# Kernel tuning notes

Measured on AMD Instinct MI355X. Metric: run time of the kernel, lower is better.

## Reference

```python
import jax, jax.numpy as jnp
import numpy as np
from jax import lax

T, N, E = 12, 10000, 160000
C_IN, C_H, C_OUT = 32, 64, 32
EPS = 1e-5


def _glorot(key, shape):
    fan_in, fan_out = shape[-2] if len(shape) > 1 else shape[0], shape[-1]
    s = (6.0 / (fan_in + fan_out)) ** 0.5
    return jax.random.uniform(key, shape, jnp.float32, -s, s)


def setup_inputs() -> dict:
    key = jax.random.key(0)
    ks = jax.random.split(key, 16)
    inp = {
        "x": jax.random.normal(ks[0], (T, N, C_IN), jnp.float32),
        "edge_index": jax.random.randint(ks[1], (2, E), 0, N, jnp.int32),
        "edge_weight": jax.random.uniform(ks[2], (E,), jnp.float32),
        # layer 1 (input layer): in=C_IN -> C_H
        "conv_w1": _glorot(ks[3], (C_H, C_IN, 3)) * 0.1,
        "conv_b1": jnp.zeros((C_H,), jnp.float32),
        "gamma1": jnp.ones((C_H,), jnp.float32),
        "beta1": jnp.zeros((C_H,), jnp.float32),
        "gcn_w1": _glorot(ks[4], (C_H, C_H)),
        "gcn_b1": jnp.zeros((C_H,), jnp.float32),
        # layer 2 (hidden layer): C_H -> C_H
        "conv_w2": _glorot(ks[5], (C_H, C_H, 3)) * 0.1,
        "conv_b2": jnp.zeros((C_H,), jnp.float32),
        "gamma2": jnp.ones((C_H,), jnp.float32),
        "beta2": jnp.zeros((C_H,), jnp.float32),
        "gcn_w2": _glorot(ks[6], (C_H, C_H)),
        "gcn_b2": jnp.zeros((C_H,), jnp.float32),
        # output linear: C_H -> C_OUT
        "out_w": _glorot(ks[7], (C_H, C_OUT)),
        "out_b": jnp.zeros((C_OUT,), jnp.float32),
    }
    return inp


def _stgcn_layer(x, edge_index, edge_weight, cw, cb, gamma, beta, gw, gb):
    # x: [T, N, C_in]  ->  torch.stack(x).permute(1,2,0) = [N, C_in, T]
    xs = jnp.transpose(x, (1, 2, 0))
    h = lax.conv_general_dilated(xs, cw, (1,), [(1, 1)],
                                 dimension_numbers=("NCH", "OIH", "NCH"))
    h = h + cb[None, :, None]
    # InstanceNorm1d(affine) over the temporal dim
    mu = h.mean(-1, keepdims=True)
    var = ((h - mu) ** 2).mean(-1, keepdims=True)
    h = (h - mu) * lax.rsqrt(var + EPS) * gamma[None, :, None] + beta[None, :, None]
    h = jax.nn.relu(h)
    h = jnp.transpose(h, (2, 0, 1))  # [T, N, C_out]
    # GCNConv per timestep (vectorized over T)
    src, dst = edge_index[0], edge_index[1]
    n = h.shape[1]
    deg = jnp.zeros((n,), h.dtype).at[dst].add(edge_weight) + 1.0  # self-loop weight 1
    dis = lax.rsqrt(deg)
    norm = dis[src] * edge_weight * dis[dst]  # [E]
    xw = jnp.einsum("tnc,cd->tnd", h, gw)  # [T, N, C_out]
    msg = xw[:, src, :] * norm[None, :, None]  # [T, E, C_out]
    agg = jax.vmap(lambda m: jax.ops.segment_sum(m, dst, num_segments=n))(msg)
    agg = agg + (dis * dis)[None, :, None] * xw + gb  # self loop + bias
    return agg


def reference(x, edge_index, edge_weight,
              conv_w1, conv_b1, gamma1, beta1, gcn_w1, gcn_b1,
              conv_w2, conv_b2, gamma2, beta2, gcn_w2, gcn_b2,
              out_w, out_b):
    h = _stgcn_layer(x, edge_index, edge_weight,
                     conv_w1, conv_b1, gamma1, beta1, gcn_w1, gcn_b1)
    h = _stgcn_layer(h, edge_index, edge_weight,
                     conv_w2, conv_b2, gamma2, beta2, gcn_w2, gcn_b2)
    out = jnp.einsum("tnc,co->tno", h, out_w) + out_b  # per-t linear
    return out.mean(axis=0)  # [N, C_OUT]
```

## Files before the change

kernel.cpp:

```cpp
#include <hip/hip_runtime.h>
#include <hip/hip_bf16.h>
#include <stdint.h>

#define MAXDEG 64

typedef short s16x8 __attribute__((ext_vector_type(8)));
typedef short s16x4 __attribute__((ext_vector_type(4)));
typedef float f32x4 __attribute__((ext_vector_type(4)));

static __device__ __forceinline__ float us2f(unsigned short u) {
    union { float f; unsigned int i; } cv; cv.i = ((unsigned int)u) << 16; return cv.f;
}
static __device__ __forceinline__ unsigned short f2us(float f) {
    __hip_bfloat16 h = __float2bfloat16(f);
    return *(unsigned short*)&h;
}

__global__ void k_build_ell(const int* __restrict__ ei, const float* __restrict__ ew,
                            float* __restrict__ deg, unsigned* __restrict__ cnt,
                            int2* __restrict__ ell, int E)
{
    int e = blockIdx.x * 256 + threadIdx.x;
    if (e >= E) return;
    int s = ei[e], d = ei[E + e];
    float w = ew[e];
    atomicAdd(&deg[d], w);
    unsigned slot = atomicAdd(&cnt[d], 1u);
    if (slot < MAXDEG) ell[(size_t)d * MAXDEG + slot] = make_int2(s, __float_as_int(w));
}

__global__ void k_norm(int2* __restrict__ ell, const unsigned* __restrict__ cnt,
                       const float* __restrict__ deg, int N)
{
    int idx = blockIdx.x * 256 + threadIdx.x;
    if (idx >= N * MAXDEG) return;
    int n = idx >> 6;
    int s = idx & (MAXDEG - 1);
    unsigned dg = cnt[n]; if (dg > MAXDEG) dg = MAXDEG;
    if ((unsigned)s >= dg) return;
    int2 p = ell[idx];
    unsigned sx = (unsigned)p.x;
    float nrm = (sx < (unsigned)N)
        ? rsqrtf(deg[sx] + 1.0f) * __int_as_float(p.y) * rsqrtf(deg[n] + 1.0f) : 0.f;
    ell[idx] = make_int2(p.x, __float_as_int(nrm));
}

#define ACCE(NRM, V0, V1, V2)                                                          \
    a[0] = fmaf(NRM, us2f(V0.x), a[0]);  a[1] = fmaf(NRM, us2f(V0.y), a[1]);           \
    a[2] = fmaf(NRM, us2f(V0.z), a[2]);  a[3] = fmaf(NRM, us2f(V0.w), a[3]);           \
    a[4] = fmaf(NRM, us2f(V1.x), a[4]);  a[5] = fmaf(NRM, us2f(V1.y), a[5]);           \
    a[6] = fmaf(NRM, us2f(V1.z), a[6]);  a[7] = fmaf(NRM, us2f(V1.w), a[7]);           \
    a[8] = fmaf(NRM, us2f(V2.x), a[8]);  a[9] = fmaf(NRM, us2f(V2.y), a[9]);           \
    a[10] = fmaf(NRM, us2f(V2.z), a[10]); a[11] = fmaf(NRM, us2f(V2.w), a[11]);

#define EDGE_GATHER(P)                                                      \
    {                                                                       \
        unsigned sx = (unsigned)(P).x;                                      \
        if (sx >= (unsigned)N) sx = 0;          \
        float nrm = __int_as_float((P).y);                                  \
        const unsigned short* qp = xw_in + (size_t)sx * 768 + L * 4;        \
        ushort4 w0 = *(const ushort4*)qp;                                   \
        ushort4 w1 = *(const ushort4*)(qp + 256);                           \
        ushort4 w2 = *(const ushort4*)(qp + 512);                           \
        ACCE(nrm, w0, w1, w2)                                               \
    }

template<int CIN>
__global__ __launch_bounds__(512, 4) void k_layer_a(
    const float* __restrict__ x_in,
    const float* __restrict__ cw,
    const float* __restrict__ gm, const float* __restrict__ bt,
    const float* __restrict__ gw,
    unsigned short* __restrict__ xw_out, int N)
{
    constexpr int KT   = CIN / 32;
    constexpr int WSTR = (CIN == 64) ? 72 : 40;
    __shared__ __align__(16) short WT[3 * 64 * WSTR];
    __shared__ __align__(16) short gwT[64 * 72];
    __shared__ __align__(16) short xh[8][14 * 72];

    const int tid = threadIdx.x;
    const int nn = tid >> 6;
    const int c = tid & 63;
    const int m = c & 15;
    const int q = c >> 4;
    const int mrow = (m < 12) ? m : 11;
    int n = blockIdx.x * 8 + nn;
    if (n >= N) n = N - 1;

    for (int g = tid; g < 3 * 64 * CIN; g += 512) {
        int kk = g / (64 * CIN);
        int r = g - kk * 64 * CIN;
        int cc = r / CIN, ci = r - cc * CIN;
        WT[kk * (64 * WSTR) + cc * WSTR + ci] = (short)f2us(cw[(cc * CIN + ci) * 3 + kk]);
    }
    for (int g = tid; g < 4096; g += 512) {
        int cc = g >> 6, d = g & 63;
        gwT[d * 72 + cc] = (short)f2us(gw[g]);
    }
    #pragma unroll
    for (int it = 0; it < (12 * CIN) / 64; ++it) {
        int i = it * 64 + c;
        int t = i / CIN, ci = i - t * CIN;
        xh[nn][(t + 1) * 72 + ci] = (short)f2us(x_in[((size_t)t * N + n) * CIN + ci]);
    }
    if (c < CIN) { xh[nn][c] = 0; xh[nn][13 * 72 + c] = 0; }
    __syncthreads();

    f32x4 acc[4];
    #pragma unroll
    for (int nt = 0; nt < 4; ++nt) acc[nt] = (f32x4){0.f, 0.f, 0.f, 0.f};
    #pragma unroll
    for (int kk = 0; kk < 3; ++kk) {
        #pragma unroll
        for (int kt = 0; kt < KT; ++kt) {
            s16x8 aA = *(const s16x8*)&xh[nn][(mrow + kk) * 72 + kt * 32 + q * 8];
            #pragma unroll
            for (int nt = 0; nt < 4; ++nt) {
                s16x8 bB = *(const s16x8*)&WT[kk * (64 * WSTR) + (nt * 16 + m) * WSTR + kt * 32 + q * 8];
                acc[nt] = __builtin_amdgcn_mfma_f32_16x16x32_bf16(aA, bB, acc[nt], 0, 0, 0);
            }
        }
    }

    #pragma unroll
    for (int nt = 0; nt < 4; ++nt) {
        float s  = acc[nt][0] + acc[nt][1] + acc[nt][2] + acc[nt][3];
        float s2 = acc[nt][0] * acc[nt][0] + acc[nt][1] * acc[nt][1]
                 + acc[nt][2] * acc[nt][2] + acc[nt][3] * acc[nt][3];
        if (q == 3) { s = 0.f; s2 = 0.f; }
        s  += __shfl_xor(s, 16);  s  += __shfl_xor(s, 32);
        s2 += __shfl_xor(s2, 16); s2 += __shfl_xor(s2, 32);
        const float mu  = s * (1.f / 12.f);
        const float var = s2 * (1.f / 12.f) - mu * mu;
        const float scn = rsqrtf(var + 1e-5f) * gm[nt * 16 + m];
        const float sbn = bt[nt * 16 + m];
        if (q < 3) {
            #pragma unroll
            for (int reg = 0; reg < 4; ++reg) {
                float h = fmaf(acc[nt][reg] - mu, scn, sbn);
                h = h > 0.f ? h : 0.f;
                xh[nn][(q * 4 + reg) * 72 + nt * 16 + m] = (short)f2us(h);
            }
        }
    }

    s16x8 a2[2];
    #pragma unroll
    for (int kt2 = 0; kt2 < 2; ++kt2)
        a2[kt2] = *(const s16x8*)&xh[nn][mrow * 72 + kt2 * 32 + q * 8];
    f32x4 acc2[4];
    #pragma unroll
    for (int nt = 0; nt < 4; ++nt) acc2[nt] = (f32x4){0.f, 0.f, 0.f, 0.f};
    #pragma unroll
    for (int nt = 0; nt < 4; ++nt) {
        #pragma unroll
        for (int kt2 = 0; kt2 < 2; ++kt2) {
            s16x8 b2 = *(const s16x8*)&gwT[(nt * 16 + m) * 72 + kt2 * 32 + q * 8];
            acc2[nt] = __builtin_amdgcn_mfma_f32_16x16x32_bf16(a2[kt2], b2, acc2[nt], 0, 0, 0);
        }
    }

    unsigned short* dst = xw_out + (size_t)n * 768;
    if (q < 3) {
        #pragma unroll
        for (int nt = 0; nt < 4; ++nt)
            #pragma unroll
            for (int reg = 0; reg < 4; ++reg)
                dst[(q * 4 + reg) * 64 + nt * 16 + m] = f2us(acc2[nt][reg]);
    }
}

__global__ __launch_bounds__(512, 4) void k_gather_a(
    const unsigned short* __restrict__ xw_in,
    const int2* __restrict__ ell, const unsigned* __restrict__ cnt,
    const float* __restrict__ deg, const float* __restrict__ gb,
    const float* __restrict__ cw,
    const float* __restrict__ gm, const float* __restrict__ bt,
    const float* __restrict__ gw,
    unsigned short* __restrict__ rowmean, int N)
{
    constexpr int WSTR = 72;
    __shared__ __align__(16) short WT[3 * 64 * WSTR];
    __shared__ __align__(16) short gwT[64 * 72];
    __shared__ __align__(16) short xh[8][14 * 72];

    const int tid = threadIdx.x;
    const int nn = tid >> 6;
    const int L = tid & 63;
    const int m = L & 15;
    const int q = L >> 4;
    const int mrow = (m < 12) ? m : 11;
    int n = blockIdx.x * 8 + nn;
    if (n >= N) n = N - 1;

    for (int g = tid; g < 3 * 64 * 64; g += 512) {
        int kk = g >> 12;
        int r = g & 4095;
        int cc = r >> 6, ci = r & 63;
        WT[kk * (64 * WSTR) + cc * WSTR + ci] = (short)f2us(cw[(cc * 64 + ci) * 3 + kk]);
    }
    for (int g = tid; g < 4096; g += 512) {
        int cc = g >> 6, d = g & 63;
        gwT[d * 72 + cc] = (short)f2us(gw[g]);
    }
    xh[nn][L] = 0; xh[nn][13 * 72 + L] = 0;
    __syncthreads();

    const float dn = rsqrtf(deg[n] + 1.0f);
    const float d2 = dn * dn;
    float a[12];
    {
        const unsigned short* self = xw_in + (size_t)n * 768 + L * 4;
        ushort4 v0 = *(const ushort4*)self;
        ushort4 v1 = *(const ushort4*)(self + 256);
        ushort4 v2 = *(const ushort4*)(self + 512);
        const int c0 = (L * 4) & 63;
        const float g0 = gb[c0], g1 = gb[c0 + 1], g2 = gb[c0 + 2], g3 = gb[c0 + 3];
        a[0] = fmaf(d2, us2f(v0.x), g0); a[1] = fmaf(d2, us2f(v0.y), g1);
        a[2] = fmaf(d2, us2f(v0.z), g2); a[3] = fmaf(d2, us2f(v0.w), g3);
        a[4] = fmaf(d2, us2f(v1.x), g0); a[5] = fmaf(d2, us2f(v1.y), g1);
        a[6] = fmaf(d2, us2f(v1.z), g2); a[7] = fmaf(d2, us2f(v1.w), g3);
        a[8] = fmaf(d2, us2f(v2.x), g0); a[9] = fmaf(d2, us2f(v2.y), g1);
        a[10] = fmaf(d2, us2f(v2.z), g2); a[11] = fmaf(d2, us2f(v2.w), g3);
    }
    unsigned dg = cnt[n]; if (dg > MAXDEG) dg = MAXDEG;
    const int2* row = ell + (size_t)n * MAXDEG;
    unsigned e = 0;
    for (; e + 4 <= dg; e += 4) {
        int2 p0 = row[e], p1 = row[e + 1], p2 = row[e + 2], p3 = row[e + 3];
        EDGE_GATHER(p0) EDGE_GATHER(p1) EDGE_GATHER(p2) EDGE_GATHER(p3)
    }
    for (; e < dg; ++e) { int2 p0 = row[e]; EDGE_GATHER(p0) }

    #pragma unroll
    for (int j = 0; j < 3; ++j) {
        s16x4 s4 = { (short)f2us(a[j * 4 + 0]), (short)f2us(a[j * 4 + 1]),
                     (short)f2us(a[j * 4 + 2]), (short)f2us(a[j * 4 + 3]) };
        *(s16x4*)&xh[nn][(j * 4 + q + 1) * 72 + ((L * 4) & 63)] = s4;
    }

    f32x4 acc[4];
    #pragma unroll
    for (int nt = 0; nt < 4; ++nt) acc[nt] = (f32x4){0.f, 0.f, 0.f, 0.f};
    #pragma unroll
    for (int kk = 0; kk < 3; ++kk) {
        #pragma unroll
        for (int kt = 0; kt < 2; ++kt) {
            s16x8 aA = *(const s16x8*)&xh[nn][(mrow + kk) * 72 + kt * 32 + q * 8];
            #pragma unroll
            for (int nt = 0; nt < 4; ++nt) {
                s16x8 bB = *(const s16x8*)&WT[kk * (64 * WSTR) + (nt * 16 + m) * WSTR + kt * 32 + q * 8];
                acc[nt] = __builtin_amdgcn_mfma_f32_16x16x32_bf16(aA, bB, acc[nt], 0, 0, 0);
            }
        }
    }

    #pragma unroll
    for (int nt = 0; nt < 4; ++nt) {
        float s  = acc[nt][0] + acc[nt][1] + acc[nt][2] + acc[nt][3];
        float s2 = acc[nt][0] * acc[nt][0] + acc[nt][1] * acc[nt][1]
                 + acc[nt][2] * acc[nt][2] + acc[nt][3] * acc[nt][3];
        if (q == 3) { s = 0.f; s2 = 0.f; }
        s  += __shfl_xor(s, 16);  s  += __shfl_xor(s, 32);
        s2 += __shfl_xor(s2, 16); s2 += __shfl_xor(s2, 32);
        const float mu  = s * (1.f / 12.f);
        const float var = s2 * (1.f / 12.f) - mu * mu;
        const float scn = rsqrtf(var + 1e-5f) * gm[nt * 16 + m];
        const float sbn = bt[nt * 16 + m];
        if (q < 3) {
            #pragma unroll
            for (int reg = 0; reg < 4; ++reg) {
                float h = fmaf(acc[nt][reg] - mu, scn, sbn);
                h = h > 0.f ? h : 0.f;
                xh[nn][(q * 4 + reg) * 72 + nt * 16 + m] = (short)f2us(h);
            }
        }
    }

    s16x8 a2[2];
    #pragma unroll
    for (int kt2 = 0; kt2 < 2; ++kt2)
        a2[kt2] = *(const s16x8*)&xh[nn][mrow * 72 + kt2 * 32 + q * 8];
    f32x4 acc2[4];
    #pragma unroll
    for (int nt = 0; nt < 4; ++nt) acc2[nt] = (f32x4){0.f, 0.f, 0.f, 0.f};
    #pragma unroll
    for (int nt = 0; nt < 4; ++nt) {
        #pragma unroll
        for (int kt2 = 0; kt2 < 2; ++kt2) {
            s16x8 b2 = *(const s16x8*)&gwT[(nt * 16 + m) * 72 + kt2 * 32 + q * 8];
            acc2[nt] = __builtin_amdgcn_mfma_f32_16x16x32_bf16(a2[kt2], b2, acc2[nt], 0, 0, 0);
        }
    }

    #pragma unroll
    for (int nt = 0; nt < 4; ++nt) {
        float pm = (q < 3) ? (acc2[nt][0] + acc2[nt][1] + acc2[nt][2] + acc2[nt][3]) : 0.f;
        pm += __shfl_xor(pm, 16); pm += __shfl_xor(pm, 32);
        if (q == 0)
            rowmean[(size_t)n * 64 + nt * 16 + m] = f2us(pm * (1.f / 12.f));
    }
}

__global__ __launch_bounds__(256) void k_final(
    const unsigned short* __restrict__ rowmean, const int2* __restrict__ ell,
    const unsigned* __restrict__ cnt, const float* __restrict__ deg,
    const float* __restrict__ gb,
    const float* __restrict__ ow, const float* __restrict__ ob,
    float* __restrict__ dout, int N)
{
    __shared__ __align__(16) float hbuf[4][64];
    const int tid = threadIdx.x;
    const int nn = tid >> 6, L = tid & 63;
    int n = blockIdx.x * 4 + nn;
    if (n >= N) n = N - 1;
    const float dn = rsqrtf(deg[n] + 1.0f);
    const float d2 = dn * dn;

    float a = fmaf(d2, us2f(rowmean[(size_t)n * 64 + L]), gb[L]);

    unsigned dg = cnt[n]; if (dg > MAXDEG) dg = MAXDEG;
    const int2* row = ell + (size_t)n * MAXDEG;
    unsigned e = 0;
    for (; e + 8 <= dg; e += 8) {
        #pragma unroll
        for (int i = 0; i < 8; ++i) {
            int2 p = row[e + i];
            unsigned sx = (unsigned)p.x;
            if (sx >= (unsigned)N) sx = 0;
            a = fmaf(__int_as_float(p.y), us2f(rowmean[(size_t)sx * 64 + L]), a);
        }
    }
    for (; e < dg; ++e) {
        int2 p = row[e];
        unsigned sx = (unsigned)p.x;
        if (sx >= (unsigned)N) sx = 0;
        a = fmaf(__int_as_float(p.y), us2f(rowmean[(size_t)sx * 64 + L]), a);
    }

    hbuf[nn][L] = a;
    __syncthreads();
    if (L < 32) {
        float oa = ob[L];
        #pragma unroll
        for (int cc = 0; cc < 64; ++cc)
            oa = fmaf(hbuf[nn][cc], ow[cc * 32 + L], oa);
        dout[(size_t)n * 32 + L] = oa;
    }
}

extern "C" void kernel_launch(void* const* d_in, const int* in_sizes, int n_in,
                              void* d_out, int out_size, void* d_ws, size_t ws_size,
                              hipStream_t stream)
{
    const float* x   = (const float*)d_in[0];
    const int*   ei  = (const int*)d_in[1];
    const float* ew  = (const float*)d_in[2];
    const float* cw1 = (const float*)d_in[3];
    const float* gm1 = (const float*)d_in[5];
    const float* bt1 = (const float*)d_in[6];
    const float* gw1 = (const float*)d_in[7];
    const float* gb1 = (const float*)d_in[8];
    const float* cw2 = (const float*)d_in[9];
    const float* gm2 = (const float*)d_in[11];
    const float* bt2 = (const float*)d_in[12];
    const float* gw2 = (const float*)d_in[13];
    const float* gb2 = (const float*)d_in[14];
    const float* ow  = (const float*)d_in[15];
    const float* ob  = (const float*)d_in[16];

    const int N = in_sizes[0] / (12 * 32);
    const int E = in_sizes[2];

    char* p0 = (char*)d_ws;
    char* p = p0;
    float* deg = (float*)p;          p += (size_t)N * 4;
    unsigned* cnt = (unsigned*)p;    p += (size_t)N * 4;
    p = (char*)(((uintptr_t)p + 255) & ~(uintptr_t)255);
    int2* ell = (int2*)p;            p += (size_t)N * MAXDEG * 8;
    p = (char*)(((uintptr_t)p + 255) & ~(uintptr_t)255);
    unsigned short* bufXW1 = (unsigned short*)p; p += (size_t)N * 768 * 2;
    unsigned short* rowmean = (unsigned short*)p; p += (size_t)N * 64 * 2;

    const size_t need = (size_t)(p - p0);
    if (ws_size < need) {
        hipMemsetAsync(d_out, 0, (size_t)out_size * 4, stream);
        return;
    }

    hipMemsetAsync(deg, 0, (size_t)N * 8, stream);

    const int eb  = (E + 255) / 256;
    const int nb8 = (N + 7) / 8;
    const int nb4 = (N + 3) / 4;
    k_build_ell<<<eb, 256, 0, stream>>>(ei, ew, deg, cnt, ell, E);
    k_norm<<<(N * MAXDEG + 255) / 256, 256, 0, stream>>>(ell, cnt, deg, N);

    k_layer_a<32><<<nb8, 512, 0, stream>>>(x, cw1, gm1, bt1, gw1, bufXW1, N);
    k_gather_a<<<nb8, 512, 0, stream>>>(bufXW1, ell, cnt, deg, gb1,
                                        cw2, gm2, bt2, gw2, rowmean, N);
    k_final<<<nb4, 256, 0, stream>>>(rowmean, ell, cnt, deg, gb2, ow, ob, (float*)d_out, N);
}
```

Baseline: 191.7 us.

## Split gather edges across two waves per node and broadcast ELL entries via readlane

k_gather_a now gives each node two waves. They split the edge list by parity, combine partial sums through shared memory, and split the MFMA output tiles between them. Edge indices and norms are loaded once per lane and broadcast with readlane, in both the gather and final kernels. k_layer_a goes to 1024-thread blocks covering 16 nodes, with float2 input loads. The aim is more parallelism and latency hiding on the memory-bound gather, paid for by extra block-wide barriers and more shared memory.

```diff
diff --git a/kernel.cpp b/kernel.cpp
--- a/kernel.cpp
+++ b/kernel.cpp
@@ -53,20 +53,20 @@
     a[8] = fmaf(NRM, us2f(V2.x), a[8]);  a[9] = fmaf(NRM, us2f(V2.y), a[9]);           \
     a[10] = fmaf(NRM, us2f(V2.z), a[10]); a[11] = fmaf(NRM, us2f(V2.w), a[11]);
 
-#define EDGE_GATHER(P)                                                      \
-    {                                                                       \
-        unsigned sx = (unsigned)(P).x;                                      \
-        if (sx >= (unsigned)N) sx = 0;          \
-        float nrm = __int_as_float((P).y);                                  \
-        const unsigned short* qp = xw_in + (size_t)sx * 768 + L * 4;        \
-        ushort4 w0 = *(const ushort4*)qp;                                   \
-        ushort4 w1 = *(const ushort4*)(qp + 256);                           \
-        ushort4 w2 = *(const ushort4*)(qp + 512);                           \
-        ACCE(nrm, w0, w1, w2)                                               \
+#define EDGE_G(EIDX)                                                                   \
+    {                                                                                  \
+        unsigned sx = (unsigned)__builtin_amdgcn_readlane(pl.x, (int)(EIDX));          \
+        float nrm = __int_as_float(__builtin_amdgcn_readlane(pl.y, (int)(EIDX)));      \
+        if (sx >= (unsigned)N) sx = 0;                     \
+        const unsigned short* qp = xw_in + (size_t)sx * 768 + L * 4;                   \
+        ushort4 w0 = *(const ushort4*)qp;                                              \
+        ushort4 w1 = *(const ushort4*)(qp + 256);                                      \
+        ushort4 w2 = *(const ushort4*)(qp + 512);                                      \
+        ACCE(nrm, w0, w1, w2)                                                          \
     }
 
 template<int CIN>
-__global__ __launch_bounds__(512, 4) void k_layer_a(
+__global__ __launch_bounds__(1024, 8) void k_layer_a(
     const float* __restrict__ x_in,
     const float* __restrict__ cw,
     const float* __restrict__ gm, const float* __restrict__ bt,
@@ -77,7 +77,7 @@
     constexpr int WSTR = (CIN == 64) ? 72 : 40;
     __shared__ __align__(16) short WT[3 * 64 * WSTR];
     __shared__ __align__(16) short gwT[64 * 72];
-    __shared__ __align__(16) short xh[8][14 * 72];
+    __shared__ __align__(16) short xh[16][14 * 72];
 
     const int tid = threadIdx.x;
     const int nn = tid >> 6;
@@ -85,24 +85,26 @@
     const int m = c & 15;
     const int q = c >> 4;
     const int mrow = (m < 12) ? m : 11;
-    int n = blockIdx.x * 8 + nn;
+    int n = blockIdx.x * 16 + nn;
     if (n >= N) n = N - 1;
 
-    for (int g = tid; g < 3 * 64 * CIN; g += 512) {
+    for (int g = tid; g < 3 * 64 * CIN; g += 1024) {
         int kk = g / (64 * CIN);
         int r = g - kk * 64 * CIN;
         int cc = r / CIN, ci = r - cc * CIN;
         WT[kk * (64 * WSTR) + cc * WSTR + ci] = (short)f2us(cw[(cc * CIN + ci) * 3 + kk]);
     }
-    for (int g = tid; g < 4096; g += 512) {
+    for (int g = tid; g < 4096; g += 1024) {
         int cc = g >> 6, d = g & 63;
         gwT[d * 72 + cc] = (short)f2us(gw[g]);
     }
     #pragma unroll
-    for (int it = 0; it < (12 * CIN) / 64; ++it) {
-        int i = it * 64 + c;
-        int t = i / CIN, ci = i - t * CIN;
-        xh[nn][(t + 1) * 72 + ci] = (short)f2us(x_in[((size_t)t * N + n) * CIN + ci]);
+    for (int it = 0; it < (12 * CIN) / 128; ++it) {
+        int i2 = it * 128 + c * 2;
+        int t = i2 / CIN, ci = i2 - t * CIN;
+        float2 xv = *(const float2*)&x_in[((size_t)t * N + n) * CIN + ci];
+        xh[nn][(t + 1) * 72 + ci]     = (short)f2us(xv.x);
+        xh[nn][(t + 1) * 72 + ci + 1] = (short)f2us(xv.y);
     }
     if (c < CIN) { xh[nn][c] = 0; xh[nn][13 * 72 + c] = 0; }
     __syncthreads();
@@ -138,9 +140,9 @@
         if (q < 3) {
             #pragma unroll
             for (int reg = 0; reg < 4; ++reg) {
-                float h = fmaf(acc[nt][reg] - mu, scn, sbn);
-                h = h > 0.f ? h : 0.f;
-                xh[nn][(q * 4 + reg) * 72 + nt * 16 + m] = (short)f2us(h);
+                float hv = fmaf(acc[nt][reg] - mu, scn, sbn);
+                hv = hv > 0.f ? hv : 0.f;
+                xh[nn][(q * 4 + reg) * 72 + nt * 16 + m] = (short)f2us(hv);
             }
         }
     }
@@ -171,7 +173,7 @@
     }
 }
 
-__global__ __launch_bounds__(512, 4) void k_gather_a(
+__global__ __launch_bounds__(1024, 8) void k_gather_a(
     const unsigned short* __restrict__ xw_in,
     const int2* __restrict__ ell, const unsigned* __restrict__ cnt,
     const float* __restrict__ deg, const float* __restrict__ gb,
@@ -184,9 +186,12 @@
     __shared__ __align__(16) short WT[3 * 64 * WSTR];
     __shared__ __align__(16) short gwT[64 * 72];
     __shared__ __align__(16) short xh[8][14 * 72];
+    __shared__ __align__(16) f32x4 pbuf[8][3][64];
 
     const int tid = threadIdx.x;
-    const int nn = tid >> 6;
+    const int wid = tid >> 6;
+    const int nn = wid >> 1;
+    const int h  = wid & 1;
     const int L = tid & 63;
     const int m = L & 15;
     const int q = L >> 4;
@@ -194,23 +199,27 @@
     int n = blockIdx.x * 8 + nn;
     if (n >= N) n = N - 1;
 
-    for (int g = tid; g < 3 * 64 * 64; g += 512) {
+    for (int g = tid; g < 3 * 64 * 64; g += 1024) {
         int kk = g >> 12;
         int r = g & 4095;
         int cc = r >> 6, ci = r & 63;
         WT[kk * (64 * WSTR) + cc * WSTR + ci] = (short)f2us(cw[(cc * 64 + ci) * 3 + kk]);
     }
-    for (int g = tid; g < 4096; g += 512) {
+    for (int g = tid; g < 4096; g += 1024) {
         int cc = g >> 6, d = g & 63;
         gwT[d * 72 + cc] = (short)f2us(gw[g]);
     }
-    xh[nn][L] = 0; xh[nn][13 * 72 + L] = 0;
+    if (h == 0) { xh[nn][L] = 0; xh[nn][13 * 72 + L] = 0; }
     __syncthreads();
 
     const float dn = rsqrtf(deg[n] + 1.0f);
     const float d2 = dn * dn;
+    const int2* row = ell + (size_t)n * MAXDEG;
+    int2 pl = row[L];
+    unsigned dg = cnt[n]; if (dg > MAXDEG) dg = MAXDEG;
+
     float a[12];
-    {
+    if (h == 0) {
         const unsigned short* self = xw_in + (size_t)n * 768 + L * 4;
         ushort4 v0 = *(const ushort4*)self;
         ushort4 v1 = *(const ushort4*)(self + 256);
@@ -223,44 +232,62 @@
         a[6] = fmaf(d2, us2f(v1.z), g2); a[7] = fmaf(d2, us2f(v1.w), g3);
         a[8] = fmaf(d2, us2f(v2.x), g0); a[9] = fmaf(d2, us2f(v2.y), g1);
         a[10] = fmaf(d2, us2f(v2.z), g2); a[11] = fmaf(d2, us2f(v2.w), g3);
-    }
-    unsigned dg = cnt[n]; if (dg > MAXDEG) dg = MAXDEG;
-    const int2* row = ell + (size_t)n * MAXDEG;
-    unsigned e = 0;
-    for (; e + 4 <= dg; e += 4) {
-        int2 p0 = row[e], p1 = row[e + 1], p2 = row[e + 2], p3 = row[e + 3];
-        EDGE_GATHER(p0) EDGE_GATHER(p1) EDGE_GATHER(p2) EDGE_GATHER(p3)
-    }
-    for (; e < dg; ++e) { int2 p0 = row[e]; EDGE_GATHER(p0) }
-
-    #pragma unroll
-    for (int j = 0; j < 3; ++j) {
-        s16x4 s4 = { (short)f2us(a[j * 4 + 0]), (short)f2us(a[j * 4 + 1]),
-                     (short)f2us(a[j * 4 + 2]), (short)f2us(a[j * 4 + 3]) };
-        *(s16x4*)&xh[nn][(j * 4 + q + 1) * 72 + ((L * 4) & 63)] = s4;
-    }
-
-    f32x4 acc[4];
-    #pragma unroll
-    for (int nt = 0; nt < 4; ++nt) acc[nt] = (f32x4){0.f, 0.f, 0.f, 0.f};
+    } else {
+        #pragma unroll
+        for (int j = 0; j < 12; ++j) a[j] = 0.f;
+    }
+
+    unsigned e = (unsigned)h;
+    for (; e + 6 < dg; e += 8) {
+        EDGE_G(e) EDGE_G(e + 2) EDGE_G(e + 4) EDGE_G(e + 6)
+    }
+    for (; e < dg; e += 2) { EDGE_G(e) }
+
+    if (h == 1) {
+        #pragma unroll
+        for (int g = 0; g < 3; ++g)
+            pbuf[nn][g][L] = (f32x4){a[4 * g], a[4 * g + 1], a[4 * g + 2], a[4 * g + 3]};
+    }
+    __syncthreads();
+    if (h == 0) {
+        #pragma unroll
+        for (int g = 0; g < 3; ++g) {
+            f32x4 t = pbuf[nn][g][L];
+            a[4 * g]     += t[0]; a[4 * g + 1] += t[1];
+            a[4 * g + 2] += t[2]; a[4 * g + 3] += t[3];
+        }
+        #pragma unroll
+        for (int j = 0; j < 3; ++j) {
+            s16x4 s4 = { (short)f2us(a[j * 4 + 0]), (short)f2us(a[j * 4 + 1]),
+                         (short)f2us(a[j * 4 + 2]), (short)f2us(a[j * 4 + 3]) };
+            *(s16x4*)&xh[nn][(j * 4 + q + 1) * 72 + ((L * 4) & 63)] = s4;
+        }
+    }
+    __syncthreads();
+
+    f32x4 acc[2];
+    acc[0] = (f32x4){0.f, 0.f, 0.f, 0.f};
+    acc[1] = (f32x4){0.f, 0.f, 0.f, 0.f};
     #pragma unroll
     for (int kk = 0; kk < 3; ++kk) {
         #pragma unroll
         for (int kt = 0; kt < 2; ++kt) {
             s16x8 aA = *(const s16x8*)&xh[nn][(mrow + kk) * 72 + kt * 32 + q * 8];
             #pragma unroll
-            for (int nt = 0; nt < 4; ++nt) {
+            for (int u = 0; u < 2; ++u) {
+                const int nt = h * 2 + u;
                 s16x8 bB = *(const s16x8*)&WT[kk * (64 * WSTR) + (nt * 16 + m) * WSTR + kt * 32 + q * 8];
-                acc[nt] = __builtin_amdgcn_mfma_f32_16x16x32_bf16(aA, bB, acc[nt], 0, 0, 0);
+                acc[u] = __builtin_amdgcn_mfma_f32_16x16x32_bf16(aA, bB, acc[u], 0, 0, 0);
             }
         }
     }
 
     #pragma unroll
-    for (int nt = 0; nt < 4; ++nt) {
-        float s  = acc[nt][0] + acc[nt][1] + acc[nt][2] + acc[nt][3];
-        float s2 = acc[nt][0] * acc[nt][0] + acc[nt][1] * acc[nt][1]
-                 + acc[nt][2] * acc[nt][2] + acc[nt][3] * acc[nt][3];
+    for (int u = 0; u < 2; ++u) {
+        const int nt = h * 2 + u;
+        float s  = acc[u][0] + acc[u][1] + acc[u][2] + acc[u][3];
+        float s2 = acc[u][0] * acc[u][0] + acc[u][1] * acc[u][1]
+                 + acc[u][2] * acc[u][2] + acc[u][3] * acc[u][3];
         if (q == 3) { s = 0.f; s2 = 0.f; }
         s  += __shfl_xor(s, 16);  s  += __shfl_xor(s, 32);
         s2 += __shfl_xor(s2, 16); s2 += __shfl_xor(s2, 32);
@@ -271,37 +298,48 @@
         if (q < 3) {
             #pragma unroll
             for (int reg = 0; reg < 4; ++reg) {
-                float h = fmaf(acc[nt][reg] - mu, scn, sbn);
-                h = h > 0.f ? h : 0.f;
-                xh[nn][(q * 4 + reg) * 72 + nt * 16 + m] = (short)f2us(h);
+                float hv = fmaf(acc[u][reg] - mu, scn, sbn);
+                hv = hv > 0.f ? hv : 0.f;
+                xh[nn][(q * 4 + reg) * 72 + nt * 16 + m] = (short)f2us(hv);
             }
         }
     }
+    __syncthreads();
 
     s16x8 a2[2];
     #pragma unroll
     for (int kt2 = 0; kt2 < 2; ++kt2)
         a2[kt2] = *(const s16x8*)&xh[nn][mrow * 72 + kt2 * 32 + q * 8];
-    f32x4 acc2[4];
-    #pragma unroll
-    for (int nt = 0; nt < 4; ++nt) acc2[nt] = (f32x4){0.f, 0.f, 0.f, 0.f};
-    #pragma unroll
-    for (int nt = 0; nt < 4; ++nt) {
+    f32x4 acc2[2];
+    acc2[0] = (f32x4){0.f, 0.f, 0.f, 0.f};
+    acc2[1] = (f32x4){0.f, 0.f, 0.f, 0.f};
+    #pragma unroll
+    for (int u = 0; u < 2; ++u) {
+        const int nt = h * 2 + u;
         #pragma unroll
         for (int kt2 = 0; kt2 < 2; ++kt2) {
             s16x8 b2 = *(const s16x8*)&gwT[(nt * 16 + m) * 72 + kt2 * 32 + q * 8];
-            acc2[nt] = __builtin_amdgcn_mfma_f32_16x16x32_bf16(a2[kt2], b2, acc2[nt], 0, 0, 0);
-        }
-    }
-
-    #pragma unroll
-    for (int nt = 0; nt < 4; ++nt) {
-        float pm = (q < 3) ? (acc2[nt][0] + acc2[nt][1] + acc2[nt][2] + acc2[nt][3]) : 0.f;
+            acc2[u] = __builtin_amdgcn_mfma_f32_16x16x32_bf16(a2[kt2], b2, acc2[u], 0, 0, 0);
+        }
+    }
+
+    #pragma unroll
+    for (int u = 0; u < 2; ++u) {
+        const int nt = h * 2 + u;
+        float pm = (q < 3) ? (acc2[u][0] + acc2[u][1] + acc2[u][2] + acc2[u][3]) : 0.f;
         pm += __shfl_xor(pm, 16); pm += __shfl_xor(pm, 32);
         if (q == 0)
             rowmean[(size_t)n * 64 + nt * 16 + m] = f2us(pm * (1.f / 12.f));
     }
 }
+
+#define FIN_E(EIDX)                                                                    \
+    {                                                                                  \
+        unsigned sx = (unsigned)__builtin_amdgcn_readlane(pl.x, (int)(EIDX));          \
+        float nrm = __int_as_float(__builtin_amdgcn_readlane(pl.y, (int)(EIDX)));      \
+        if (sx >= (unsigned)N) sx = 0;                                                 \
+        a = fmaf(nrm, us2f(rowmean[(size_t)sx * 64 + L]), a);                          \
+    }
 
 __global__ __launch_bounds__(256) void k_final(
     const unsigned short* __restrict__ rowmean, const int2* __restrict__ ell,
@@ -318,26 +356,18 @@
     const float dn = rsqrtf(deg[n] + 1.0f);
     const float d2 = dn * dn;
 
+    const int2* row = ell + (size_t)n * MAXDEG;
+    int2 pl = row[L];
+    unsigned dg = cnt[n]; if (dg > MAXDEG) dg = MAXDEG;
+
     float a = fmaf(d2, us2f(rowmean[(size_t)n * 64 + L]), gb[L]);
 
-    unsigned dg = cnt[n]; if (dg > MAXDEG) dg = MAXDEG;
-    const int2* row = ell + (size_t)n * MAXDEG;
     unsigned e = 0;
-    for (; e + 8 <= dg; e += 8) {
-        #pragma unroll
-        for (int i = 0; i < 8; ++i) {
-            int2 p = row[e + i];
-            unsigned sx = (unsigned)p.x;
-            if (sx >= (unsigned)N) sx = 0;
-            a = fmaf(__int_as_float(p.y), us2f(rowmean[(size_t)sx * 64 + L]), a);
-        }
-    }
-    for (; e < dg; ++e) {
-        int2 p = row[e];
-        unsigned sx = (unsigned)p.x;
-        if (sx >= (unsigned)N) sx = 0;
-        a = fmaf(__int_as_float(p.y), us2f(rowmean[(size_t)sx * 64 + L]), a);
-    }
+    for (; e + 7 < dg; e += 8) {
+        FIN_E(e)     FIN_E(e + 1) FIN_E(e + 2) FIN_E(e + 3)
+        FIN_E(e + 4) FIN_E(e + 5) FIN_E(e + 6) FIN_E(e + 7)
+    }
+    for (; e < dg; ++e) { FIN_E(e) }
 
     hbuf[nn][L] = a;
     __syncthreads();
@@ -391,14 +421,15 @@
 
     hipMemsetAsync(deg, 0, (size_t)N * 8, stream);
 
-    const int eb  = (E + 255) / 256;
-    const int nb8 = (N + 7) / 8;
-    const int nb4 = (N + 3) / 4;
+    const int eb   = (E + 255) / 256;
+    const int nb16 = (N + 15) / 16;
+    const int nb8  = (N + 7) / 8;
+    const int nb4  = (N + 3) / 4;
     k_build_ell<<<eb, 256, 0, stream>>>(ei, ew, deg, cnt, ell, E);
     k_norm<<<(N * MAXDEG + 255) / 256, 256, 0, stream>>>(ell, cnt, deg, N);
 
-    k_layer_a<32><<<nb8, 512, 0, stream>>>(x, cw1, gm1, bt1, gw1, bufXW1, N);
-    k_gather_a<<<nb8, 512, 0, stream>>>(bufXW1, ell, cnt, deg, gb1,
-                                        cw2, gm2, bt2, gw2, rowmean, N);
+    k_layer_a<32><<<nb16, 1024, 0, stream>>>(x, cw1, gm1, bt1, gw1, bufXW1, N);
+    k_gather_a<<<nb8, 1024, 0, stream>>>(bufXW1, ell, cnt, deg, gb1,
+                                         cw2, gm2, bt2, gw2, rowmean, N);
     k_final<<<nb4, 256, 0, stream>>>(rowmean, ell, cnt, deg, gb2, ow, ob, (float*)d_out, N);
 }
```

Measured after the change: 193.9 us. About the same (+1.1%).

## Preload ELL rows per wavefront, batch gathers, and enlarge layer-A blocks

Applied to the files above, without the earlier changes.

The gather and final kernels now load a node's whole ELL row once with one coalesced per-lane load and broadcast each edge with readlane, instead of issuing scalar row loads per edge. The layer-2 gather issues eight edges' loads before accumulating so more memory requests are in flight, and it hoists the self-feature and degree loads above the weight-staging sync. Layer A moves to 1024-thread blocks covering 16 nodes, which amortizes weight staging across more nodes, and reads x as float2. In exchange, register pressure rises and the larger blocks could lower occupancy.

```diff
diff --git a/kernel.cpp b/kernel.cpp
--- a/kernel.cpp
+++ b/kernel.cpp
@@ -53,20 +53,8 @@
     a[8] = fmaf(NRM, us2f(V2.x), a[8]);  a[9] = fmaf(NRM, us2f(V2.y), a[9]);           \
     a[10] = fmaf(NRM, us2f(V2.z), a[10]); a[11] = fmaf(NRM, us2f(V2.w), a[11]);
 
-#define EDGE_GATHER(P)                                                      \
-    {                                                                       \
-        unsigned sx = (unsigned)(P).x;                                      \
-        if (sx >= (unsigned)N) sx = 0;          \
-        float nrm = __int_as_float((P).y);                                  \
-        const unsigned short* qp = xw_in + (size_t)sx * 768 + L * 4;        \
-        ushort4 w0 = *(const ushort4*)qp;                                   \
-        ushort4 w1 = *(const ushort4*)(qp + 256);                           \
-        ushort4 w2 = *(const ushort4*)(qp + 512);                           \
-        ACCE(nrm, w0, w1, w2)                                               \
-    }
-
 template<int CIN>
-__global__ __launch_bounds__(512, 4) void k_layer_a(
+__global__ __launch_bounds__(1024, 4) void k_layer_a(
     const float* __restrict__ x_in,
     const float* __restrict__ cw,
     const float* __restrict__ gm, const float* __restrict__ bt,
@@ -77,7 +65,7 @@
     constexpr int WSTR = (CIN == 64) ? 72 : 40;
     __shared__ __align__(16) short WT[3 * 64 * WSTR];
     __shared__ __align__(16) short gwT[64 * 72];
-    __shared__ __align__(16) short xh[8][14 * 72];
+    __shared__ __align__(16) short xh[16][14 * 72];
 
     const int tid = threadIdx.x;
     const int nn = tid >> 6;
@@ -85,24 +73,26 @@
     const int m = c & 15;
     const int q = c >> 4;
     const int mrow = (m < 12) ? m : 11;
-    int n = blockIdx.x * 8 + nn;
+    int n = blockIdx.x * 16 + nn;
     if (n >= N) n = N - 1;
 
-    for (int g = tid; g < 3 * 64 * CIN; g += 512) {
+    for (int g = tid; g < 3 * 64 * CIN; g += 1024) {
         int kk = g / (64 * CIN);
         int r = g - kk * 64 * CIN;
         int cc = r / CIN, ci = r - cc * CIN;
         WT[kk * (64 * WSTR) + cc * WSTR + ci] = (short)f2us(cw[(cc * CIN + ci) * 3 + kk]);
     }
-    for (int g = tid; g < 4096; g += 512) {
+    for (int g = tid; g < 4096; g += 1024) {
         int cc = g >> 6, d = g & 63;
         gwT[d * 72 + cc] = (short)f2us(gw[g]);
     }
     #pragma unroll
-    for (int it = 0; it < (12 * CIN) / 64; ++it) {
-        int i = it * 64 + c;
-        int t = i / CIN, ci = i - t * CIN;
-        xh[nn][(t + 1) * 72 + ci] = (short)f2us(x_in[((size_t)t * N + n) * CIN + ci]);
+    for (int it = 0; it < (12 * CIN) / 128; ++it) {
+        int i2 = it * 128 + c * 2;
+        int t = i2 / CIN, ci = i2 - t * CIN;
+        float2 xv = *(const float2*)&x_in[((size_t)t * N + n) * CIN + ci];
+        xh[nn][(t + 1) * 72 + ci]     = (short)f2us(xv.x);
+        xh[nn][(t + 1) * 72 + ci + 1] = (short)f2us(xv.y);
     }
     if (c < CIN) { xh[nn][c] = 0; xh[nn][13 * 72 + c] = 0; }
     __syncthreads();
@@ -138,9 +128,9 @@
         if (q < 3) {
             #pragma unroll
             for (int reg = 0; reg < 4; ++reg) {
-                float h = fmaf(acc[nt][reg] - mu, scn, sbn);
-                h = h > 0.f ? h : 0.f;
-                xh[nn][(q * 4 + reg) * 72 + nt * 16 + m] = (short)f2us(h);
+                float hv = fmaf(acc[nt][reg] - mu, scn, sbn);
+                hv = hv > 0.f ? hv : 0.f;
+                xh[nn][(q * 4 + reg) * 72 + nt * 16 + m] = (short)f2us(hv);
             }
         }
     }
@@ -194,6 +184,16 @@
     int n = blockIdx.x * 8 + nn;
     if (n >= N) n = N - 1;
 
+    const int2* row = ell + (size_t)n * MAXDEG;
+    int2 pl = row[L];
+    unsigned dg = cnt[n]; if (dg > MAXDEG) dg = MAXDEG;
+    const float dn = rsqrtf(deg[n] + 1.0f);
+    const float d2 = dn * dn;
+    const unsigned short* self = xw_in + (size_t)n * 768 + L * 4;
+    ushort4 v0 = *(const ushort4*)self;
+    ushort4 v1 = *(const ushort4*)(self + 256);
+    ushort4 v2 = *(const ushort4*)(self + 512);
+
     for (int g = tid; g < 3 * 64 * 64; g += 512) {
         int kk = g >> 12;
         int r = g & 4095;
@@ -207,14 +207,8 @@
     xh[nn][L] = 0; xh[nn][13 * 72 + L] = 0;
     __syncthreads();
 
-    const float dn = rsqrtf(deg[n] + 1.0f);
-    const float d2 = dn * dn;
     float a[12];
     {
-        const unsigned short* self = xw_in + (size_t)n * 768 + L * 4;
-        ushort4 v0 = *(const ushort4*)self;
-        ushort4 v1 = *(const ushort4*)(self + 256);
-        ushort4 v2 = *(const ushort4*)(self + 512);
         const int c0 = (L * 4) & 63;
         const float g0 = gb[c0], g1 = gb[c0 + 1], g2 = gb[c0 + 2], g3 = gb[c0 + 3];
         a[0] = fmaf(d2, us2f(v0.x), g0); a[1] = fmaf(d2, us2f(v0.y), g1);
@@ -224,14 +218,51 @@
         a[8] = fmaf(d2, us2f(v2.x), g0); a[9] = fmaf(d2, us2f(v2.y), g1);
         a[10] = fmaf(d2, us2f(v2.z), g2); a[11] = fmaf(d2, us2f(v2.w), g3);
     }
-    unsigned dg = cnt[n]; if (dg > MAXDEG) dg = MAXDEG;
-    const int2* row = ell + (size_t)n * MAXDEG;
+
     unsigned e = 0;
-    for (; e + 4 <= dg; e += 4) {
-        int2 p0 = row[e], p1 = row[e + 1], p2 = row[e + 2], p3 = row[e + 3];
-        EDGE_GATHER(p0) EDGE_GATHER(p1) EDGE_GATHER(p2) EDGE_GATHER(p3)
-    }
-    for (; e < dg; ++e) { int2 p0 = row[e]; EDGE_GATHER(p0) }
+    for (; e + 8 <= dg; e += 8) {
+        ushort4 B0[8], B1[8], B2[8];
+        float NR[8];
+        #pragma unroll
+        for (int i = 0; i < 8; ++i) {
+            unsigned sx = (unsigned)__builtin_amdgcn_readlane(pl.x, (int)(e + i));
+            NR[i] = __int_as_float(__builtin_amdgcn_readlane(pl.y, (int)(e + i)));
+            if (sx >= (unsigned)N) sx = 0;
+            const unsigned short* qp = xw_in + (size_t)sx * 768 + L * 4;
+            B0[i] = *(const ushort4*)qp;
+            B1[i] = *(const ushort4*)(qp + 256);
+            B2[i] = *(const ushort4*)(qp + 512);
+        }
+        #pragma unroll
+        for (int i = 0; i < 8; ++i) { ACCE(NR[i], B0[i], B1[i], B2[i]) }
+    }
+    if (e + 4 <= dg) {
+        ushort4 B0[4], B1[4], B2[4];
+        float NR[4];
+        #pragma unroll
+        for (int i = 0; i < 4; ++i) {
+            unsigned sx = (unsigned)__builtin_amdgcn_readlane(pl.x, (int)(e + i));
+            NR[i] = __int_as_float(__builtin_amdgcn_readlane(pl.y, (int)(e + i)));
+            if (sx >= (unsigned)N) sx = 0;
+            const unsigned short* qp = xw_in + (size_t)sx * 768 + L * 4;
+            B0[i] = *(const ushort4*)qp;
+            B1[i] = *(const ushort4*)(qp + 256);
+            B2[i] = *(const ushort4*)(qp + 512);
+        }
+        #pragma unroll
+        for (int i = 0; i < 4; ++i) { ACCE(NR[i], B0[i], B1[i], B2[i]) }
+        e += 4;
+    }
+    for (; e < dg; ++e) {
+        unsigned sx = (unsigned)__builtin_amdgcn_readlane(pl.x, (int)e);
+        float nr = __int_as_float(__builtin_amdgcn_readlane(pl.y, (int)e));
+        if (sx >= (unsigned)N) sx = 0;
+        const unsigned short* qp = xw_in + (size_t)sx * 768 + L * 4;
+        ushort4 w0 = *(const ushort4*)qp;
+        ushort4 w1 = *(const ushort4*)(qp + 256);
+        ushort4 w2 = *(const ushort4*)(qp + 512);
+        ACCE(nr, w0, w1, w2)
+    }
 
     #pragma unroll
     for (int j = 0; j < 3; ++j) {
@@ -271,9 +302,9 @@
         if (q < 3) {
             #pragma unroll
             for (int reg = 0; reg < 4; ++reg) {
-                float h = fmaf(acc[nt][reg] - mu, scn, sbn);
-                h = h > 0.f ? h : 0.f;
-                xh[nn][(q * 4 + reg) * 72 + nt * 16 + m] = (short)f2us(h);
+                float hv = fmaf(acc[nt][reg] - mu, scn, sbn);
+                hv = hv > 0.f ? hv : 0.f;
+                xh[nn][(q * 4 + reg) * 72 + nt * 16 + m] = (short)f2us(hv);
             }
         }
     }
@@ -302,6 +333,14 @@
             rowmean[(size_t)n * 64 + nt * 16 + m] = f2us(pm * (1.f / 12.f));
     }
 }
+
+#define FIN_E(EIDX)                                                                    \
+    {                                                                                  \
+        unsigned sx = (unsigned)__builtin_amdgcn_readlane(pl.x, (int)(EIDX));          \
+        float nrm = __int_as_float(__builtin_amdgcn_readlane(pl.y, (int)(EIDX)));      \
+        if (sx >= (unsigned)N) sx = 0;                                                 \
+        a = fmaf(nrm, us2f(rowmean[(size_t)sx * 64 + L]), a);                          \
+    }
 
 __global__ __launch_bounds__(256) void k_final(
     const unsigned short* __restrict__ rowmean, const int2* __restrict__ ell,
@@ -318,26 +357,18 @@
     const float dn = rsqrtf(deg[n] + 1.0f);
     const float d2 = dn * dn;
 
+    const int2* row = ell + (size_t)n * MAXDEG;
+    int2 pl = row[L];
+    unsigned dg = cnt[n]; if (dg > MAXDEG) dg = MAXDEG;
+
     float a = fmaf(d2, us2f(rowmean[(size_t)n * 64 + L]), gb[L]);
 
-    unsigned dg = cnt[n]; if (dg > MAXDEG) dg = MAXDEG;
-    const int2* row = ell + (size_t)n * MAXDEG;
     unsigned e = 0;
-    for (; e + 8 <= dg; e += 8) {
-        #pragma unroll
-        for (int i = 0; i < 8; ++i) {
-            int2 p = row[e + i];
-            unsigned sx = (unsigned)p.x;
-            if (sx >= (unsigned)N) sx = 0;
-            a = fmaf(__int_as_float(p.y), us2f(rowmean[(size_t)sx * 64 + L]), a);
-        }
-    }
-    for (; e < dg; ++e) {
-        int2 p = row[e];
-        unsigned sx = (unsigned)p.x;
-        if (sx >= (unsigned)N) sx = 0;
-        a = fmaf(__int_as_float(p.y), us2f(rowmean[(size_t)sx * 64 + L]), a);
-    }
+    for (; e + 7 < dg; e += 8) {
+        FIN_E(e)     FIN_E(e + 1) FIN_E(e + 2) FIN_E(e + 3)
+        FIN_E(e + 4) FIN_E(e + 5) FIN_E(e + 6) FIN_E(e + 7)
+    }
+    for (; e < dg; ++e) { FIN_E(e) }
 
     hbuf[nn][L] = a;
     __syncthreads();
@@ -391,13 +422,14 @@
 
     hipMemsetAsync(deg, 0, (size_t)N * 8, stream);
 
-    const int eb  = (E + 255) / 256;
-    const int nb8 = (N + 7) / 8;
-    const int nb4 = (N + 3) / 4;
+    const int eb   = (E + 255) / 256;
+    const int nb16 = (N + 15) / 16;
+    const int nb8  = (N + 7) / 8;
+    const int nb4  = (N + 3) / 4;
     k_build_ell<<<eb, 256, 0, stream>>>(ei, ew, deg, cnt, ell, E);
     k_norm<<<(N * MAXDEG + 255) / 256, 256, 0, stream>>>(ell, cnt, deg, N);
 
-    k_layer_a<32><<<nb8, 512, 0, stream>>>(x, cw1, gm1, bt1, gw1, bufXW1, N);
+    k_layer_a<32><<<nb16, 1024, 0, stream>>>(x, cw1, gm1, bt1, gw1, bufXW1, N);
     k_gather_a<<<nb8, 512, 0, stream>>>(bufXW1, ell, cnt, deg, gb1,
                                         cw2, gm2, bt2, gw2, rowmean, N);
     k_final<<<nb4, 256, 0, stream>>>(rowmean, ell, cnt, deg, gb2, ow, ob, (float*)d_out, N);
```

After: 184.9 us. 1.04x faster.
